# Optimization experiments

Hardware: AMD Instinct MI355X
Metric: run time of the kernel (lower is better)

Reference implementation:

```python
import jax, jax.numpy as jnp
import numpy as np

B, S, D = 4, 2048, 768
H = 12
HD = D // H  # 64


def setup_inputs() -> dict:
    key = jax.random.key(0)
    k1, k2, k3 = jax.random.split(key, 3)
    return {
        "hidden_states": jax.random.normal(k1, (B, S, D), dtype=jnp.float32),
        "W_attn": jax.random.normal(k2, (D, 3 * D), dtype=jnp.float32) * 0.02,
        "b_attn": jnp.zeros((3 * D,), dtype=jnp.float32),
        "W_proj": jax.random.normal(k3, (D, D), dtype=jnp.float32) * 0.02,
        "b_proj": jnp.zeros((D,), dtype=jnp.float32),
    }


def reference(hidden_states, W_attn, b_attn, W_proj, b_proj):
    # Conv1D c_attn: x @ W + b -> [B, S, 3D]
    qkv = hidden_states @ W_attn + b_attn
    q, k, v = jnp.split(qkv, 3, axis=-1)

    def split_heads(t):
        # [B, S, D] -> [B, H, S, HD]
        return t.reshape(B, S, H, HD).transpose(0, 2, 1, 3)

    q, k, v = split_heads(q), split_heads(k), split_heads(v)

    # attn_weights = q @ k^T / sqrt(head_dim); NOTE: this module variant applies
    # no causal mask when attention_mask is None (faithful to source _attn).
    scale = jnp.asarray(HD, dtype=q.dtype) ** 0.5
    scores = jnp.einsum("bhqd,bhkd->bhqk", q, k) / scale
    weights = jax.nn.softmax(scores, axis=-1)

    attn = jnp.einsum("bhqk,bhkd->bhqd", weights, v)
    # merge heads -> [B, S, D]
    attn = attn.transpose(0, 2, 1, 3).reshape(B, S, D)
    # Conv1D c_proj
    out = attn @ W_proj + b_proj
    return out
```

## Files before the change

### kernel.cpp

```cpp
#include <hip/hip_runtime.h>

typedef short short8 __attribute__((ext_vector_type(8)));
typedef float f32x4 __attribute__((ext_vector_type(4)));
typedef float f32x16 __attribute__((ext_vector_type(16)));

__device__ __forceinline__ unsigned short f2bf(float f){
  union { float f; unsigned int u; } x; x.f = f;
  unsigned int r = x.u + 0x7fffu + ((x.u >> 16) & 1u);
  return (unsigned short)(r >> 16);
}

__device__ __forceinline__ void gload_lds16(const void* g, void* l){
  __builtin_amdgcn_global_load_lds(
      (const __attribute__((address_space(1))) void*)g,
      (__attribute__((address_space(3))) void*)l, 16, 0, 0);
}

__device__ __forceinline__ unsigned int cvtpk_bf16(float lo, float hi){
  unsigned int r;
  asm("v_cvt_pk_bf16_f32 %0, %1, %2" : "=v"(r) : "v"(lo), "v"(hi));
  return r;
}

__global__ __launch_bounds__(256) void cast_f32_bf16(const float* __restrict__ in,
                                                     unsigned short* __restrict__ out, int n4){
  int i = blockIdx.x * blockDim.x + threadIdx.x;
  const int stride = gridDim.x * blockDim.x;
  for (; i < n4; i += stride){
    float4 v = ((const float4*)in)[i];
    ushort4 o;
    o.x = f2bf(v.x); o.y = f2bf(v.y); o.z = f2bf(v.z); o.w = f2bf(v.w);
    ((ushort4*)out)[i] = o;
  }
}

__global__ __launch_bounds__(256) void transpose_to_bf16(const float* __restrict__ W,
                                                         unsigned short* __restrict__ WT,
                                                         int K, int N){
  __shared__ float tile[64][68];
  const int n0 = blockIdx.x * 64, k0 = blockIdx.y * 64;
  const int t = threadIdx.x;
  const int qn = (t & 15) * 4;
  #pragma unroll
  for (int i = 0; i < 4; ++i){
    const int kk = (t >> 4) + i * 16;
    float4 v = *(const float4*)&W[(size_t)(k0 + kk) * N + n0 + qn];
    tile[kk][qn + 0] = v.x; tile[kk][qn + 1] = v.y;
    tile[kk][qn + 2] = v.z; tile[kk][qn + 3] = v.w;
  }
  __syncthreads();
  const int qk = (t & 15) * 4;
  #pragma unroll
  for (int i = 0; i < 4; ++i){
    const int nn = (t >> 4) + i * 16;
    ushort4 o;
    o.x = f2bf(tile[qk + 0][nn]); o.y = f2bf(tile[qk + 1][nn]);
    o.z = f2bf(tile[qk + 2][nn]); o.w = f2bf(tile[qk + 3][nn]);
    *(ushort4*)&WT[(size_t)(n0 + nn) * K + k0 + qk] = o;
  }
}

template<int EPI>
__global__ __launch_bounds__(256) void gemm_bf16(const unsigned short* __restrict__ A,
                                                 const unsigned short* __restrict__ Bt,
                                                 const float* __restrict__ bias,
                                                 void* __restrict__ outp){
  __shared__ unsigned short As[2][128 * 32];
  __shared__ unsigned short Bs[2][128 * 32];
  const int tid = threadIdx.x;
  const int wave = tid >> 6, lane = tid & 63;
  const int g = lane >> 4, l15 = lane & 15;
  const int wr = wave >> 1, wc = wave & 1;
  const int m0 = blockIdx.y * 128, n0 = blockIdx.x * 128;

  f32x4 acc[4][4] = {};

  auto stage = [&](int bi, int kt){
    const int k0 = kt * 32;
    #pragma unroll
    for (int c = 0; c < 2; ++c){
      const int z = c * 4096 + tid * 16;
      const int r = z >> 6;
      const int ys = (z & 63) ^ ((r & 3) << 4);
      gload_lds16((const char*)A + ((size_t)(m0 + r) * 768 + k0) * 2 + ys,
                  (char*)&As[bi][0] + c * 4096 + wave * 1024);
      gload_lds16((const char*)Bt + ((size_t)(n0 + r) * 768 + k0) * 2 + ys,
                  (char*)&Bs[bi][0] + c * 4096 + wave * 1024);
    }
  };

  stage(0, 0);
  for (int kt = 0; kt < 24; ++kt){
    __syncthreads();
    if (kt + 1 < 24) stage((kt + 1) & 1, kt + 1);
    const char* Ab = (const char*)&As[kt & 1][0];
    const char* Bb = (const char*)&Bs[kt & 1][0];
    short8 a[4], b[4];
    #pragma unroll
    for (int mt = 0; mt < 4; ++mt){
      const int row = wr * 64 + mt * 16 + l15;
      a[mt] = *(const short8*)(Ab + row * 64 + ((g * 16) ^ ((row & 3) << 4)));
    }
    #pragma unroll
    for (int nt = 0; nt < 4; ++nt){
      const int row = wc * 64 + nt * 16 + l15;
      b[nt] = *(const short8*)(Bb + row * 64 + ((g * 16) ^ ((row & 3) << 4)));
    }
    #pragma unroll
    for (int mt = 0; mt < 4; ++mt)
      #pragma unroll
      for (int nt = 0; nt < 4; ++nt)
        acc[mt][nt] = __builtin_amdgcn_mfma_f32_16x16x32_bf16(a[mt], b[nt], acc[mt][nt], 0, 0, 0);
  }

  if (EPI == 0){
    unsigned short* qkv = (unsigned short*)outp;
    #pragma unroll
    for (int nt = 0; nt < 4; ++nt){
      const int n = n0 + wc * 64 + nt * 16 + l15;
      const int which = n / 768;
      const float bs = bias[n];
      if (which == 2){
        const int hd = n & 63;
        const int head = (n - 1536) >> 6;
        #pragma unroll
        for (int mt = 0; mt < 4; ++mt){
          const int m = m0 + wr * 64 + mt * 16 + 4 * g;
          const int bb = m >> 11, sidx = m & 2047;
          unsigned short* dst = qkv + (size_t)2 * 6291456 +
                                ((size_t)(bb * 12 + head) * 64 + hd) * 2048 + sidx;
          #pragma unroll
          for (int rp = 0; rp < 2; ++rp){
            const unsigned int lo = f2bf(acc[mt][nt][2 * rp] + bs);
            const unsigned int hi = f2bf(acc[mt][nt][2 * rp + 1] + bs);
            *(unsigned int*)(dst + 2 * rp) = lo | (hi << 16);
          }
        }
      } else {
        const int h2 = (n - which * 768) >> 6;
        const int hd = n & 63;
        const float sc = (which == 0) ? 0.125f : 1.0f;
        #pragma unroll
        for (int mt = 0; mt < 4; ++mt)
          #pragma unroll
          for (int r = 0; r < 4; ++r){
            const int m = m0 + wr * 64 + mt * 16 + 4 * g + r;
            const int bb = m >> 11, sidx = m & 2047;
            qkv[(size_t)which * 6291456u +
                ((((size_t)bb * 12 + h2) * 2048 + sidx) * 64 + hd)] = f2bf((acc[mt][nt][r] + bs) * sc);
          }
      }
    }
  } else {
    float* out = (float*)outp;
    #pragma unroll
    for (int mt = 0; mt < 4; ++mt)
      #pragma unroll
      for (int nt = 0; nt < 4; ++nt){
        const int n = n0 + wc * 64 + nt * 16 + l15;
        const float bs = bias[n];
        #pragma unroll
        for (int r = 0; r < 4; ++r){
          const int m = m0 + wr * 64 + mt * 16 + 4 * g + r;
          out[(size_t)m * 768 + n] = acc[mt][nt][r] + bs;
        }
      }
  }
}

__global__ __launch_bounds__(256) void attn_fwd2(const unsigned short* __restrict__ qw,
                                                 const unsigned short* __restrict__ kw,
                                                 const unsigned short* __restrict__ vtw,
                                                 unsigned short* __restrict__ aout){
  __shared__ unsigned short Ks[2][64 * 64];
  __shared__ unsigned short Vs[2][64 * 64];
  __shared__ float bcast[4][32];
  const int tid = threadIdx.x;
  const int wave = tid >> 6, lane = tid & 63;
  const int h = lane >> 5, ql = lane & 31;
  const int bh = blockIdx.y;
  const int q0 = blockIdx.x * 128 + wave * 32;
  const size_t base = (size_t)bh * 2048 * 64;

  short8 qf[4];
  #pragma unroll
  for (int c = 0; c < 4; ++c)
    qf[c] = *(const short8*)(qw + base + (size_t)(q0 + ql) * 64 + c * 16 + h * 8);

  f32x16 acc[2] = {};
  float mreg = -1e30f, lsum = 0.f;

  auto stageKV = [&](int bi, int t){
    #pragma unroll
    for (int c = 0; c < 2; ++c){
      const int z = c * 4096 + tid * 16;
      const int r = z >> 7, y = z & 127;
      const int ys = y ^ ((r & 7) << 4);
      gload_lds16((const char*)kw + (base + (size_t)(t * 64 + r) * 64) * 2 + ys,
                  (char*)&Ks[bi][0] + z);
      gload_lds16((const char*)vtw + (base + (size_t)r * 2048 + t * 64) * 2 + ys,
                  (char*)&Vs[bi][0] + z);
    }
  };

  stageKV(0, 0);
  __syncthreads();

  for (int t = 0; t < 32; ++t){
    const int buf = t & 1;
    if (t + 1 < 32) stageKV(buf ^ 1, t + 1);

    f32x16 s[2] = {};
    #pragma unroll
    for (int kt = 0; kt < 2; ++kt)
      #pragma unroll
      for (int c = 0; c < 4; ++c){
        const int row = kt * 32 + ql;
        short8 af = *(const short8*)((const char*)&Ks[buf][0] + row * 128 +
                                     ((c * 32 + h * 16) ^ ((row & 7) << 4)));
        s[kt] = __builtin_amdgcn_mfma_f32_32x32x16_bf16(af, qf[c], s[kt], 0, 0, 0);
      }

    float pm = s[0][0];
    #pragma unroll
    for (int kt = 0; kt < 2; ++kt)
      #pragma unroll
      for (int r = 0; r < 16; ++r) pm = fmaxf(pm, s[kt][r]);
    pm = fmaxf(pm, __shfl_xor(pm, 32));

    if (__any(pm > mreg + 8.f)){
      const float mn = fmaxf(mreg, pm);
      const float fr = __expf(mreg - mn);
      mreg = mn;
      lsum *= fr;
      if (h == 0) bcast[wave][ql] = fr;
      #pragma unroll
      for (int g4 = 0; g4 < 4; ++g4){
        float4 f4 = *(const float4*)&bcast[wave][8 * g4 + 4 * h];
        #pragma unroll
        for (int j = 0; j < 4; ++j){
          const float fj = ((const float*)&f4)[j];
          acc[0][4 * g4 + j] *= fj;
          acc[1][4 * g4 + j] *= fj;
        }
      }
    }

    float ps = 0.f;
    #pragma unroll
    for (int kt = 0; kt < 2; ++kt)
      #pragma unroll
      for (int r = 0; r < 16; ++r){
        const float p = __expf(s[kt][r] - mreg);
        s[kt][r] = p;
        ps += p;
      }
    lsum += ps;

    #pragma unroll
    for (int kt = 0; kt < 2; ++kt){
      unsigned int w0 = cvtpk_bf16(s[kt][0],  s[kt][1]),  x0 = cvtpk_bf16(s[kt][4],  s[kt][5]);
      asm("v_permlane32_swap_b32 %0, %1" : "+v"(w0), "+v"(x0));
      unsigned int w1 = cvtpk_bf16(s[kt][2],  s[kt][3]),  x1 = cvtpk_bf16(s[kt][6],  s[kt][7]);
      asm("v_permlane32_swap_b32 %0, %1" : "+v"(w1), "+v"(x1));
      unsigned int w2 = cvtpk_bf16(s[kt][8],  s[kt][9]),  x2 = cvtpk_bf16(s[kt][12], s[kt][13]);
      asm("v_permlane32_swap_b32 %0, %1" : "+v"(w2), "+v"(x2));
      unsigned int w3 = cvtpk_bf16(s[kt][10], s[kt][11]), x3 = cvtpk_bf16(s[kt][14], s[kt][15]);
      asm("v_permlane32_swap_b32 %0, %1" : "+v"(w3), "+v"(x3));
      union { unsigned int u[4]; short8 v; } pa[2];
      pa[0].u[0] = w0; pa[0].u[1] = w1; pa[0].u[2] = x0; pa[0].u[3] = x1;
      pa[1].u[0] = w2; pa[1].u[1] = w3; pa[1].u[2] = x2; pa[1].u[3] = x3;
      #pragma unroll
      for (int c2 = 0; c2 < 2; ++c2){
        const int kc = kt * 2 + c2;
        #pragma unroll
        for (int ht = 0; ht < 2; ++ht){
          const int row = ht * 32 + ql;
          short8 vb = *(const short8*)((const char*)&Vs[buf][0] + row * 128 +
                                       ((kc * 32 + h * 16) ^ ((row & 7) << 4)));
          acc[ht] = __builtin_amdgcn_mfma_f32_32x32x16_bf16(pa[c2].v, vb, acc[ht], 0, 0, 0);
        }
      }
    }

    __syncthreads();
  }

  lsum += __shfl_xor(lsum, 32);
  if (h == 0) bcast[wave][ql] = 1.0f / lsum;
  const int bb = bh / 12, hh = bh % 12;
  #pragma unroll
  for (int g4 = 0; g4 < 4; ++g4){
    float4 f4 = *(const float4*)&bcast[wave][8 * g4 + 4 * h];
    #pragma unroll
    for (int j = 0; j < 4; ++j){
      const int row = 8 * g4 + 4 * h + j;
      const float li = ((const float*)&f4)[j];
      #pragma unroll
      for (int ht = 0; ht < 2; ++ht)
        aout[(size_t)(bb * 2048 + q0 + row) * 768 + hh * 64 + ht * 32 + ql] =
            f2bf(acc[ht][4 * g4 + j] * li);
    }
  }
}

extern "C" void kernel_launch(void* const* d_in, const int* in_sizes, int n_in,
                              void* d_out, int out_size, void* d_ws, size_t ws_size,
                              hipStream_t stream){
  const float* hs = (const float*)d_in[0];
  const float* Wa = (const float*)d_in[1];
  const float* ba = (const float*)d_in[2];
  const float* Wp = (const float*)d_in[3];
  const float* bp = (const float*)d_in[4];

  char* ws = (char*)d_ws;
  unsigned short* hbf = (unsigned short*)ws;
  unsigned short* WaT = (unsigned short*)(ws + 12582912);
  unsigned short* WpT = (unsigned short*)(ws + 12582912 + 3538944);
  unsigned short* qkv = (unsigned short*)(ws + 12582912 + 3538944 + 1179648);
  unsigned short* abf = qkv + (size_t)3 * 6291456;

  cast_f32_bf16<<<dim3(2048), dim3(256), 0, stream>>>(hs, hbf, 8192 * 768 / 4);
  transpose_to_bf16<<<dim3(36, 12), dim3(256), 0, stream>>>(Wa, WaT, 768, 2304);
  transpose_to_bf16<<<dim3(12, 12), dim3(256), 0, stream>>>(Wp, WpT, 768, 768);
  gemm_bf16<0><<<dim3(18, 64), dim3(256), 0, stream>>>(hbf, WaT, ba, (void*)qkv);
  attn_fwd2<<<dim3(16, 48), dim3(256), 0, stream>>>(qkv, qkv + 6291456, qkv + (size_t)2 * 6291456, abf);
  gemm_bf16<1><<<dim3(6, 64), dim3(256), 0, stream>>>(abf, WpT, bp, d_out);
}
```

Measured before the change: 187.5 us.

## Use exp2 softmax with folded log2e scale, MFMA priority, and dedicated projection GEMM

```diff
diff --git a/kernel.cpp b/kernel.cpp
--- a/kernel.cpp
+++ b/kernel.cpp
@@ -1,6 +1,7 @@
 #include <hip/hip_runtime.h>
 
 typedef short short8 __attribute__((ext_vector_type(8)));
+typedef float f32x2 __attribute__((ext_vector_type(2)));
 typedef float f32x4 __attribute__((ext_vector_type(4)));
 typedef float f32x16 __attribute__((ext_vector_type(16)));
 
@@ -20,6 +21,12 @@
   unsigned int r;
   asm("v_cvt_pk_bf16_f32 %0, %1, %2" : "=v"(r) : "v"(lo), "v"(hi));
   return r;
+}
+
+__device__ __forceinline__ f32x2 pk_add(f32x2 a, f32x2 b){
+  f32x2 d;
+  asm("v_pk_add_f32 %0, %1, %2" : "=v"(d) : "v"(a), "v"(b));
+  return d;
 }
 
 __global__ __launch_bounds__(256) void cast_f32_bf16(const float* __restrict__ in,
@@ -139,7 +146,7 @@
       } else {
         const int h2 = (n - which * 768) >> 6;
         const int hd = n & 63;
-        const float sc = (which == 0) ? 0.125f : 1.0f;
+        const float sc = (which == 0) ? 0.18033688f : 1.0f;
         #pragma unroll
         for (int mt = 0; mt < 4; ++mt)
           #pragma unroll
@@ -151,24 +158,78 @@
           }
       }
     }
-  } else {
-    float* out = (float*)outp;
-    #pragma unroll
-    for (int mt = 0; mt < 4; ++mt)
-      #pragma unroll
-      for (int nt = 0; nt < 4; ++nt){
-        const int n = n0 + wc * 64 + nt * 16 + l15;
-        const float bs = bias[n];
-        #pragma unroll
-        for (int r = 0; r < 4; ++r){
-          const int m = m0 + wr * 64 + mt * 16 + 4 * g + r;
-          out[(size_t)m * 768 + n] = acc[mt][nt][r] + bs;
-        }
-      }
-  }
-}
-
-__global__ __launch_bounds__(256) void attn_fwd2(const unsigned short* __restrict__ qw,
+  }
+}
+
+__global__ __launch_bounds__(256) void gemm_proj(const unsigned short* __restrict__ A,
+                                                 const unsigned short* __restrict__ Bt,
+                                                 const float* __restrict__ bias,
+                                                 float* __restrict__ out){
+  __shared__ unsigned short As[2][128 * 32];
+  __shared__ unsigned short Bs[2][64 * 32];
+  const int tid = threadIdx.x;
+  const int wave = tid >> 6, lane = tid & 63;
+  const int g = lane >> 4, l15 = lane & 15;
+  const int m0 = blockIdx.y * 128, n0 = blockIdx.x * 64;
+
+  f32x4 acc[2][4] = {};
+
+  auto stage = [&](int bi, int kt){
+    const int k0 = kt * 32;
+    #pragma unroll
+    for (int c = 0; c < 2; ++c){
+      const int z = c * 4096 + tid * 16;
+      const int r = z >> 6;
+      const int ys = (z & 63) ^ ((r & 3) << 4);
+      gload_lds16((const char*)A + ((size_t)(m0 + r) * 768 + k0) * 2 + ys,
+                  (char*)&As[bi][0] + c * 4096 + wave * 1024);
+    }
+    const int z = tid * 16;
+    const int r = z >> 6;
+    const int ys = (z & 63) ^ ((r & 3) << 4);
+    gload_lds16((const char*)Bt + ((size_t)(n0 + r) * 768 + k0) * 2 + ys,
+                (char*)&Bs[bi][0] + wave * 1024);
+  };
+
+  stage(0, 0);
+  for (int kt = 0; kt < 24; ++kt){
+    __syncthreads();
+    if (kt + 1 < 24) stage((kt + 1) & 1, kt + 1);
+    const char* Ab = (const char*)&As[kt & 1][0];
+    const char* Bb = (const char*)&Bs[kt & 1][0];
+    short8 a[2], b[4];
+    #pragma unroll
+    for (int mt = 0; mt < 2; ++mt){
+      const int row = wave * 32 + mt * 16 + l15;
+      a[mt] = *(const short8*)(Ab + row * 64 + ((g * 16) ^ ((row & 3) << 4)));
+    }
+    #pragma unroll
+    for (int nt = 0; nt < 4; ++nt){
+      const int row = nt * 16 + l15;
+      b[nt] = *(const short8*)(Bb + row * 64 + ((g * 16) ^ ((row & 3) << 4)));
+    }
+    #pragma unroll
+    for (int mt = 0; mt < 2; ++mt)
+      #pragma unroll
+      for (int nt = 0; nt < 4; ++nt)
+        acc[mt][nt] = __builtin_amdgcn_mfma_f32_16x16x32_bf16(a[mt], b[nt], acc[mt][nt], 0, 0, 0);
+  }
+
+  #pragma unroll
+  for (int mt = 0; mt < 2; ++mt)
+    #pragma unroll
+    for (int nt = 0; nt < 4; ++nt){
+      const int n = n0 + nt * 16 + l15;
+      const float bs = bias[n];
+      #pragma unroll
+      for (int r = 0; r < 4; ++r){
+        const int m = m0 + wave * 32 + mt * 16 + 4 * g + r;
+        out[(size_t)m * 768 + n] = acc[mt][nt][r] + bs;
+      }
+    }
+}
+
+__global__ __launch_bounds__(256) void attn_fwd3(const unsigned short* __restrict__ qw,
                                                  const unsigned short* __restrict__ kw,
                                                  const unsigned short* __restrict__ vtw,
                                                  unsigned short* __restrict__ aout){
@@ -188,52 +249,75 @@
     qf[c] = *(const short8*)(qw + base + (size_t)(q0 + ql) * 64 + c * 16 + h * 8);
 
   f32x16 acc[2] = {};
-  float mreg = -1e30f, lsum = 0.f;
-
-  auto stageKV = [&](int bi, int t){
-    #pragma unroll
-    for (int c = 0; c < 2; ++c){
-      const int z = c * 4096 + tid * 16;
-      const int r = z >> 7, y = z & 127;
-      const int ys = y ^ ((r & 7) << 4);
-      gload_lds16((const char*)kw + (base + (size_t)(t * 64 + r) * 64) * 2 + ys,
-                  (char*)&Ks[bi][0] + z);
-      gload_lds16((const char*)vtw + (base + (size_t)r * 2048 + t * 64) * 2 + ys,
-                  (char*)&Vs[bi][0] + z);
-    }
-  };
-
-  stageKV(0, 0);
+  f32x16 minit = {};
+  float mreg = 0.f, lsum = 0.f;
+
+  int koff[2], voff[2], zz[2];
+  #pragma unroll
+  for (int c = 0; c < 2; ++c){
+    const int z = c * 4096 + tid * 16;
+    const int r = z >> 7, y = z & 127;
+    zz[c] = z;
+    koff[c] = r * 128 + (y ^ ((r & 7) << 4));
+    voff[c] = r * 4096 + (y ^ ((r & 7) << 4));
+  }
+  const char* kq = (const char*)kw + base * 2;
+  const char* vq = (const char*)vtw + base * 2;
+
+  #pragma unroll
+  for (int c = 0; c < 2; ++c){
+    gload_lds16(kq + koff[c], (char*)&Ks[0][0] + zz[c]);
+    gload_lds16(vq + voff[c], (char*)&Vs[0][0] + zz[c]);
+  }
+  kq += 8192; vq += 128;
   __syncthreads();
 
   for (int t = 0; t < 32; ++t){
     const int buf = t & 1;
-    if (t + 1 < 32) stageKV(buf ^ 1, t + 1);
-
-    f32x16 s[2] = {};
-    #pragma unroll
-    for (int kt = 0; kt < 2; ++kt)
-      #pragma unroll
-      for (int c = 0; c < 4; ++c){
-        const int row = kt * 32 + ql;
-        short8 af = *(const short8*)((const char*)&Ks[buf][0] + row * 128 +
-                                     ((c * 32 + h * 16) ^ ((row & 7) << 4)));
+    if (t + 1 < 32){
+      #pragma unroll
+      for (int c = 0; c < 2; ++c){
+        gload_lds16(kq + koff[c], (char*)&Ks[buf ^ 1][0] + zz[c]);
+        gload_lds16(vq + voff[c], (char*)&Vs[buf ^ 1][0] + zz[c]);
+      }
+      kq += 8192; vq += 128;
+    }
+
+    f32x16 s[2];
+    __builtin_amdgcn_s_setprio(1);
+    #pragma unroll
+    for (int kt = 0; kt < 2; ++kt){
+      const int row = kt * 32 + ql;
+      short8 af = *(const short8*)((const char*)&Ks[buf][0] + row * 128 +
+                                   ((h * 16) ^ ((row & 7) << 4)));
+      s[kt] = __builtin_amdgcn_mfma_f32_32x32x16_bf16(af, qf[0], minit, 0, 0, 0);
+      #pragma unroll
+      for (int c = 1; c < 4; ++c){
+        af = *(const short8*)((const char*)&Ks[buf][0] + row * 128 +
+                              ((c * 32 + h * 16) ^ ((row & 7) << 4)));
         s[kt] = __builtin_amdgcn_mfma_f32_32x32x16_bf16(af, qf[c], s[kt], 0, 0, 0);
       }
-
-    float pm = s[0][0];
-    #pragma unroll
-    for (int kt = 0; kt < 2; ++kt)
-      #pragma unroll
-      for (int r = 0; r < 16; ++r) pm = fmaxf(pm, s[kt][r]);
+    }
+    __builtin_amdgcn_s_setprio(0);
+
+    float pa = s[0][0], pb = s[1][0];
+    #pragma unroll
+    for (int r = 1; r < 15; r += 2){
+      pa = fmaxf(fmaxf(pa, s[0][r]), s[0][r + 1]);
+      pb = fmaxf(fmaxf(pb, s[1][r]), s[1][r + 1]);
+    }
+    pa = fmaxf(pa, s[0][15]); pb = fmaxf(pb, s[1][15]);
+    float pm = fmaxf(pa, pb);
     pm = fmaxf(pm, __shfl_xor(pm, 32));
 
-    if (__any(pm > mreg + 8.f)){
-      const float mn = fmaxf(mreg, pm);
-      const float fr = __expf(mreg - mn);
-      mreg = mn;
+    if (t == 0 || __any(pm > 11.5f)){
+      const float pe = (t == 0) ? pm : fmaxf(pm, 0.f);
+      mreg += pe;
+      const float fr = __builtin_amdgcn_exp2f(-pe);
       lsum *= fr;
       if (h == 0) bcast[wave][ql] = fr;
+      #pragma unroll
+      for (int r = 0; r < 16; ++r) minit[r] = -mreg;
       #pragma unroll
       for (int g4 = 0; g4 < 4; ++g4){
         float4 f4 = *(const float4*)&bcast[wave][8 * g4 + 4 * h];
@@ -244,18 +328,34 @@
           acc[1][4 * g4 + j] *= fj;
         }
       }
-    }
-
-    float ps = 0.f;
-    #pragma unroll
-    for (int kt = 0; kt < 2; ++kt)
-      #pragma unroll
-      for (int r = 0; r < 16; ++r){
-        const float p = __expf(s[kt][r] - mreg);
-        s[kt][r] = p;
-        ps += p;
-      }
-    lsum += ps;
+      #pragma unroll
+      for (int kt = 0; kt < 2; ++kt)
+        #pragma unroll
+        for (int r = 0; r < 16; ++r)
+          s[kt][r] = __builtin_amdgcn_exp2f(s[kt][r] - pe);
+    } else {
+      #pragma unroll
+      for (int kt = 0; kt < 2; ++kt)
+        #pragma unroll
+        for (int r = 0; r < 16; ++r)
+          s[kt][r] = __builtin_amdgcn_exp2f(s[kt][r]);
+    }
+
+    {
+      f32x2 a0 = pk_add(__builtin_shufflevector(s[0], s[0], 0, 1),  __builtin_shufflevector(s[0], s[0], 2, 3));
+      f32x2 a1 = pk_add(__builtin_shufflevector(s[0], s[0], 4, 5),  __builtin_shufflevector(s[0], s[0], 6, 7));
+      f32x2 a2 = pk_add(__builtin_shufflevector(s[0], s[0], 8, 9),  __builtin_shufflevector(s[0], s[0], 10, 11));
+      f32x2 a3 = pk_add(__builtin_shufflevector(s[0], s[0], 12, 13), __builtin_shufflevector(s[0], s[0], 14, 15));
+      f32x2 b0 = pk_add(__builtin_shufflevector(s[1], s[1], 0, 1),  __builtin_shufflevector(s[1], s[1], 2, 3));
+      f32x2 b1 = pk_add(__builtin_shufflevector(s[1], s[1], 4, 5),  __builtin_shufflevector(s[1], s[1], 6, 7));
+      f32x2 b2 = pk_add(__builtin_shufflevector(s[1], s[1], 8, 9),  __builtin_shufflevector(s[1], s[1], 10, 11));
+      f32x2 b3 = pk_add(__builtin_shufflevector(s[1], s[1], 12, 13), __builtin_shufflevector(s[1], s[1], 14, 15));
+      a0 = pk_add(a0, a1); a2 = pk_add(a2, a3);
+      b0 = pk_add(b0, b1); b2 = pk_add(b2, b3);
+      a0 = pk_add(a0, a2); b0 = pk_add(b0, b2);
+      a0 = pk_add(a0, b0);
+      lsum += a0[0] + a0[1];
+    }
 
     #pragma unroll
     for (int kt = 0; kt < 2; ++kt){
@@ -267,9 +367,10 @@
       asm("v_permlane32_swap_b32 %0, %1" : "+v"(w2), "+v"(x2));
       unsigned int w3 = cvtpk_bf16(s[kt][10], s[kt][11]), x3 = cvtpk_bf16(s[kt][14], s[kt][15]);
       asm("v_permlane32_swap_b32 %0, %1" : "+v"(w3), "+v"(x3));
-      union { unsigned int u[4]; short8 v; } pa[2];
-      pa[0].u[0] = w0; pa[0].u[1] = w1; pa[0].u[2] = x0; pa[0].u[3] = x1;
-      pa[1].u[0] = w2; pa[1].u[1] = w3; pa[1].u[2] = x2; pa[1].u[3] = x3;
+      union { unsigned int u[4]; short8 v; } pa2[2];
+      pa2[0].u[0] = w0; pa2[0].u[1] = w1; pa2[0].u[2] = x0; pa2[0].u[3] = x1;
+      pa2[1].u[0] = w2; pa2[1].u[1] = w3; pa2[1].u[2] = x2; pa2[1].u[3] = x3;
+      __builtin_amdgcn_s_setprio(1);
       #pragma unroll
       for (int c2 = 0; c2 < 2; ++c2){
         const int kc = kt * 2 + c2;
@@ -278,9 +379,10 @@
           const int row = ht * 32 + ql;
           short8 vb = *(const short8*)((const char*)&Vs[buf][0] + row * 128 +
                                        ((kc * 32 + h * 16) ^ ((row & 7) << 4)));
-          acc[ht] = __builtin_amdgcn_mfma_f32_32x32x16_bf16(pa[c2].v, vb, acc[ht], 0, 0, 0);
+          acc[ht] = __builtin_amdgcn_mfma_f32_32x32x16_bf16(pa2[c2].v, vb, acc[ht], 0, 0, 0);
         }
       }
+      __builtin_amdgcn_s_setprio(0);
     }
 
     __syncthreads();
@@ -324,6 +426,6 @@
   transpose_to_bf16<<<dim3(36, 12), dim3(256), 0, stream>>>(Wa, WaT, 768, 2304);
   transpose_to_bf16<<<dim3(12, 12), dim3(256), 0, stream>>>(Wp, WpT, 768, 768);
   gemm_bf16<0><<<dim3(18, 64), dim3(256), 0, stream>>>(hbf, WaT, ba, (void*)qkv);
-  attn_fwd2<<<dim3(16, 48), dim3(256), 0, stream>>>(qkv, qkv + 6291456, qkv + (size_t)2 * 6291456, abf);
-  gemm_bf16<1><<<dim3(6, 64), dim3(256), 0, stream>>>(abf, WpT, bp, d_out);
-}
+  attn_fwd3<<<dim3(16, 48), dim3(256), 0, stream>>>(qkv, qkv + 6291456, qkv + (size_t)2 * 6291456, abf);
+  gemm_proj<<<dim3(12, 64), dim3(256), 0, stream>>>(abf, WpT, bp, (float*)d_out);
+}
```

Measured after the change: 233.6 us. +24.6%, slower.
